# Optimization experiments

Measured on AMD Instinct MI355X. Metric: run time of the kernel, lower is better.

## Reference

```python
import jax, jax.numpy as jnp
import numpy as np

B = 262144   # batch
L = 50       # sequence feature length (hardcoded in source loop)
H = 1024     # fc_hidden_size
E = 256      # embedding_dim
DROP_P = 0.2


def setup_inputs() -> dict:
    key = jax.random.key(0)
    k1, k2, k3, k4 = jax.random.split(key, 4)
    seq = jax.random.normal(k1, (B, 1, L), dtype=jnp.float32)
    # emulate -1 padding after a random valid length so the early-break path is exercised
    lengths = jax.random.randint(k2, (B,), 10, L + 1)
    pad = jnp.arange(L)[None, None, :] >= lengths[:, None, None]
    seq = jnp.where(pad, jnp.float32(-1.0), seq)
    W1 = jax.random.normal(k3, (L, H), dtype=jnp.float32) * np.float32(1.0 / np.sqrt(L))
    b1 = jnp.zeros((H,), dtype=jnp.float32)
    W2 = jax.random.normal(k4, (H, E), dtype=jnp.float32) * np.float32(1.0 / np.sqrt(H))
    b2 = jnp.zeros((E,), dtype=jnp.float32)
    return {"seq": seq, "W1": W1, "b1": b1, "W2": W2, "b2": b2}


def reference(seq, W1, b1, W2, b2):
    x = seq[:, 0, :]                                   # [B, L]
    # first position equal to -1 per row (loop breaks there); L if none
    is_neg = x == jnp.float32(-1.0)
    first_neg = jnp.where(is_neg.any(axis=-1), jnp.argmax(is_neg, axis=-1), L)  # [B]
    valid = jnp.arange(L)[None, :] < first_neg[:, None]                          # [B, L]
    # per-element Bernoulli(0.2) dropout applied only before the break point
    drop = jax.random.uniform(jax.random.key(42), x.shape) < DROP_P
    x = jnp.where(drop & valid, jnp.float32(0.0), x)
    # Linear -> ReLU -> Linear, then squeeze(1) (already squeezed above)
    h = jax.nn.relu(x @ W1 + b1)                       # [B, H]
    return h @ W2 + b2                                 # [B, E]
```

## Files before the change

### kernel.cpp

```cpp
#include <hip/hip_runtime.h>


typedef __attribute__((ext_vector_type(8))) short short8;
typedef __attribute__((ext_vector_type(4))) float f32x4;

__device__ __forceinline__ unsigned short f2bf(float f) {
  unsigned u = __float_as_uint(f);
  u += 0x7fffu + ((u >> 16) & 1u);
  return (unsigned short)(u >> 16);
}

__device__ __forceinline__ unsigned rotl_(unsigned x, int d) {
  return (x << d) | (x >> (32 - d));
}

__device__ __forceinline__ bool drop_rand(unsigned j) {
  const unsigned k0 = 0u, k1 = 42u, k2 = 0x1BD11BDAu ^ 42u;
  unsigned v0 = 0u + k0;
  unsigned v1 = j + k1;
#define MIX(rot) { v0 += v1; v1 = rotl_(v1, rot); v1 ^= v0; }
  MIX(13) MIX(15) MIX(26) MIX(6)   v0 += k1; v1 += k2 + 1u;
  MIX(17) MIX(29) MIX(16) MIX(24)  v0 += k2; v1 += k0 + 2u;
  MIX(13) MIX(15) MIX(26) MIX(6)   v0 += k0; v1 += k1 + 3u;
  MIX(17) MIX(29) MIX(16) MIX(24)  v0 += k1; v1 += k2 + 4u;
  MIX(13) MIX(15) MIX(26) MIX(6)   v0 += k2; v1 += k0 + 5u;
#undef MIX
  unsigned bits = v0 ^ v1;
  float u = __uint_as_float((bits >> 9) | 0x3f800000u) - 1.0f;
  return u < 0.2f;
}

__global__ void pack_weights(const float* __restrict__ W1, const float* __restrict__ W2,
                             unsigned short* __restrict__ ws) {
  int t = blockIdx.x * 256 + threadIdx.x;
  if (t < 8192) {
    int nblk = t >> 7, kb = (t >> 6) & 1, lane = t & 63;
    int kbase = kb * 32 + ((lane >> 4) * 8);
    int col = nblk * 16 + (lane & 15);
    short8 vv;
#pragma unroll
    for (int j = 0; j < 8; ++j) {
      int k = kbase + j;
      vv[j] = (short)((k < 50) ? f2bf(W1[k * 1024 + col]) : (unsigned short)0);
    }
    *(short8*)&ws[t * 8] = vv;
  } else {
    int t2 = t - 8192;
    int c = t2 >> 11, kb = (t2 >> 10) & 1, nt = (t2 >> 6) & 15, lane = t2 & 63;
    int kbase = c * 64 + kb * 32 + ((lane >> 4) * 8);
    int e = nt * 16 + (lane & 15);
    short8 vv;
#pragma unroll
    for (int j = 0; j < 8; ++j) vv[j] = (short)f2bf(W2[(size_t)(kbase + j) * 256 + e]);
    *(short8*)&ws[65536 + t2 * 8] = vv;
  }
}

__global__ __launch_bounds__(512, 2) void mlp_fused(
    const float* __restrict__ seq, const float* __restrict__ b1,
    const float* __restrict__ b2, const unsigned short* __restrict__ ws,
    float* __restrict__ out) {
  __shared__ __align__(16) unsigned short lds_x[8192];
  __shared__ __align__(16) unsigned short lds_h[8192];
  __shared__ __align__(16) unsigned short lds_w2[16384];

  const int tid  = threadIdx.x;
  const int lane = tid & 63;
  const int wave = tid >> 6;
  const int quad = lane >> 4;
  const int l15  = lane & 15;
  const int m0   = blockIdx.x * 128;
  const unsigned short* pW1 = ws;
  const unsigned short* pW2 = ws + 65536;

  {
    int r = tid >> 2, q = tid & 3;
    int grow = m0 + r;
    const float* xrow = seq + (size_t)grow * 50;
    float xv[16];
    unsigned negm = 0;
#pragma unroll
    for (int i = 0; i < 16; ++i) {
      int l = q * 16 + i;
      float v = (l < 50) ? xrow[l] : 0.0f;
      xv[i] = v;
      if (v == -1.0f) negm |= (1u << i);
    }
    unsigned long long rm = ((unsigned long long)negm) << (q * 16);
    rm |= __shfl_xor(rm, 1);
    rm |= __shfl_xor(rm, 2);
    int fn = rm ? __builtin_ctzll(rm) : 64;
    unsigned jbase = (unsigned)grow * 50u;
#pragma unroll
    for (int g = 0; g < 2; ++g) {
      short8 vv;
#pragma unroll
      for (int i = 0; i < 8; ++i) {
        int l = q * 16 + g * 8 + i;
        float v = xv[g * 8 + i];
        if (l < fn && l < 50 && drop_rand(jbase + (unsigned)l)) v = 0.0f;
        vv[i] = (short)f2bf(v);
      }
      int kq = q * 2 + g;
      int idx = (((r >> 4) * 2 + (kq >> 2)) * 64 + (kq & 3) * 16 + (r & 15)) * 8;
      *(short8*)&lds_x[idx] = vv;
    }
  }

  f32x4 acc[4][4];
#pragma unroll
  for (int mi = 0; mi < 4; ++mi)
#pragma unroll
    for (int ni = 0; ni < 4; ++ni) acc[mi][ni] = f32x4{0.f, 0.f, 0.f, 0.f};

  const int w1m = wave >> 1, w1n = wave & 1;
  const int gm  = wave >> 2, gn  = wave & 3;

  for (int c = 0; c < 16; ++c) {
    short8 stg[4];
#pragma unroll
    for (int it = 0; it < 4; ++it)
      stg[it] = *(const short8*)&pW2[(size_t)c * 16384 + (size_t)(it * 512 + tid) * 8];

    __syncthreads();

    f32x4 hacc[2][2];
#pragma unroll
    for (int mi = 0; mi < 2; ++mi)
#pragma unroll
      for (int ni = 0; ni < 2; ++ni) hacc[mi][ni] = f32x4{0.f, 0.f, 0.f, 0.f};
#pragma unroll
    for (int kb = 0; kb < 2; ++kb) {
      short8 xa[2], wb[2];
#pragma unroll
      for (int mi = 0; mi < 2; ++mi)
        xa[mi] = *(const short8*)&lds_x[(size_t)(((w1m * 2 + mi) * 2 + kb) * 64 + lane) * 8];
#pragma unroll
      for (int ni = 0; ni < 2; ++ni)
        wb[ni] = *(const short8*)&pW1[(size_t)(((c * 4 + w1n * 2 + ni) * 2 + kb) * 64 + lane) * 8];
#pragma unroll
      for (int mi = 0; mi < 2; ++mi)
#pragma unroll
        for (int ni = 0; ni < 2; ++ni)
          hacc[mi][ni] = __builtin_amdgcn_mfma_f32_16x16x32_bf16(xa[mi], wb[ni], hacc[mi][ni], 0, 0, 0);
    }
#pragma unroll
    for (int ni = 0; ni < 2; ++ni) {
      int ntg = w1n * 2 + ni;
      int khl = ntg * 16 + l15;
      float b1v = b1[c * 64 + khl];
      int kb2 = ntg >> 1;
      int quad2 = ((ntg & 1) << 1) | (l15 >> 3);
      int jj = l15 & 7;
#pragma unroll
      for (int mi = 0; mi < 2; ++mi) {
        int mblk = w1m * 2 + mi;
#pragma unroll
        for (int r = 0; r < 4; ++r) {
          float v = fmaxf(hacc[mi][ni][r] + b1v, 0.0f);
          lds_h[(size_t)((mblk * 2 + kb2) * 64 + quad2 * 16 + quad * 4 + r) * 8 + jj] = f2bf(v);
        }
      }
    }
#pragma unroll
    for (int it = 0; it < 4; ++it)
      *(short8*)&lds_w2[(size_t)(it * 512 + tid) * 8] = stg[it];

    __syncthreads();

#pragma unroll
    for (int kb = 0; kb < 2; ++kb) {
      short8 ha[4], wb2[4];
#pragma unroll
      for (int mi = 0; mi < 4; ++mi)
        ha[mi] = *(const short8*)&lds_h[(size_t)(((gm * 4 + mi) * 2 + kb) * 64 + lane) * 8];
#pragma unroll
      for (int ni = 0; ni < 4; ++ni)
        wb2[ni] = *(const short8*)&lds_w2[(size_t)((kb * 16 + gn * 4 + ni) * 64 + lane) * 8];
#pragma unroll
      for (int mi = 0; mi < 4; ++mi)
#pragma unroll
        for (int ni = 0; ni < 4; ++ni)
          acc[mi][ni] = __builtin_amdgcn_mfma_f32_16x16x32_bf16(ha[mi], wb2[ni], acc[mi][ni], 0, 0, 0);
    }
  }

#pragma unroll
  for (int ni = 0; ni < 4; ++ni) {
    int e = (gn * 4 + ni) * 16 + l15;
    float b2v = b2[e];
#pragma unroll
    for (int mi = 0; mi < 4; ++mi) {
      int mrow = m0 + (gm * 4 + mi) * 16 + quad * 4;
#pragma unroll
      for (int r = 0; r < 4; ++r)
        out[(size_t)(mrow + r) * 256 + e] = acc[mi][ni][r] + b2v;
    }
  }
}

extern "C" void kernel_launch(void* const* d_in, const int* in_sizes, int n_in,
                              void* d_out, int out_size, void* d_ws, size_t ws_size,
                              hipStream_t stream) {
  const float* seq = (const float*)d_in[0];
  const float* W1  = (const float*)d_in[1];
  const float* b1  = (const float*)d_in[2];
  const float* W2  = (const float*)d_in[3];
  const float* b2  = (const float*)d_in[4];
  unsigned short* ws = (unsigned short*)d_ws;
  float* out = (float*)d_out;

  hipLaunchKernelGGL(pack_weights, dim3(160), dim3(256), 0, stream, W1, W2, ws);
  hipLaunchKernelGGL(mlp_fused, dim3(2048), dim3(512), 0, stream, seq, b1, b2, ws, out);
}
```

Baseline: 508.5 us.

## Keep X in registers, double-buffer H in LDS, read W2 directly from global

Each wave now keeps its own 16 input rows in registers and computes the full 64-wide hidden chunk as W1ᵀ·x, so the lds_x buffer goes away. The hidden tile is double-buffered in LDS, which cuts the per-chunk barriers from two to one. The W2 tile is no longer staged through LDS; each wave loads its W2 fragments straight from global memory and relies on L2/L1 hits. Less LDS lets the launch bounds target 4 blocks per CU, at the cost of more redundant global W2 traffic and possible register pressure from 16 accumulators.

```diff
diff --git a/kernel.cpp b/kernel.cpp
--- a/kernel.cpp
+++ b/kernel.cpp
@@ -56,145 +56,137 @@
   }
 }
 
-__global__ __launch_bounds__(512, 2) void mlp_fused(
+__global__ __launch_bounds__(512, 4) void mlp_fused(
     const float* __restrict__ seq, const float* __restrict__ b1,
     const float* __restrict__ b2, const unsigned short* __restrict__ ws,
     float* __restrict__ out) {
-  __shared__ __align__(16) unsigned short lds_x[8192];
-  __shared__ __align__(16) unsigned short lds_h[8192];
-  __shared__ __align__(16) unsigned short lds_w2[16384];
+  __shared__ __align__(16) unsigned short lds_h[2][8192];
 
   const int tid  = threadIdx.x;
   const int lane = tid & 63;
   const int wave = tid >> 6;
-  const int quad = lane >> 4;
+  const int q    = lane >> 4;
   const int l15  = lane & 15;
   const int m0   = blockIdx.x * 128;
   const unsigned short* pW1 = ws;
   const unsigned short* pW2 = ws + 65536;
 
+  short8 xb[2];
   {
-    int r = tid >> 2, q = tid & 3;
-    int grow = m0 + r;
-    const float* xrow = seq + (size_t)grow * 50;
-    float xv[16];
-    unsigned negm = 0;
-#pragma unroll
-    for (int i = 0; i < 16; ++i) {
-      int l = q * 16 + i;
-      float v = (l < 50) ? xrow[l] : 0.0f;
-      xv[i] = v;
-      if (v == -1.0f) negm |= (1u << i);
-    }
-    unsigned long long rm = ((unsigned long long)negm) << (q * 16);
-    rm |= __shfl_xor(rm, 1);
-    rm |= __shfl_xor(rm, 2);
-    int fn = rm ? __builtin_ctzll(rm) : 64;
-    unsigned jbase = (unsigned)grow * 50u;
-#pragma unroll
-    for (int g = 0; g < 2; ++g) {
+    const int row = m0 + wave * 16 + l15;
+    const float* xrow = seq + (size_t)row * 50;
+    float xv[2][8];
+    unsigned long long nm = 0ull;
+#pragma unroll
+    for (int kb = 0; kb < 2; ++kb) {
+#pragma unroll
+      for (int jp = 0; jp < 4; ++jp) {
+        const int k = kb * 32 + q * 8 + jp * 2;
+        float2 v;
+        if (k < 50) v = *(const float2*)&xrow[k];
+        else        v = make_float2(0.f, 0.f);
+        xv[kb][jp * 2]     = v.x;
+        xv[kb][jp * 2 + 1] = v.y;
+        if (v.x == -1.0f) nm |= 1ull << k;
+        if (v.y == -1.0f) nm |= 1ull << (k + 1);
+      }
+    }
+    nm |= __shfl_xor(nm, 16);
+    nm |= __shfl_xor(nm, 32);
+    const int fn   = nm ? __builtin_ctzll(nm) : 64;
+    const int kmax = fn < 50 ? fn : 50;
+    const unsigned jbase = (unsigned)row * 50u;
+#pragma unroll
+    for (int kb = 0; kb < 2; ++kb) {
       short8 vv;
 #pragma unroll
-      for (int i = 0; i < 8; ++i) {
-        int l = q * 16 + g * 8 + i;
-        float v = xv[g * 8 + i];
-        if (l < fn && l < 50 && drop_rand(jbase + (unsigned)l)) v = 0.0f;
-        vv[i] = (short)f2bf(v);
+      for (int j = 0; j < 8; ++j) {
+        const int k = kb * 32 + q * 8 + j;
+        float v = xv[kb][j];
+        if (k < kmax && drop_rand(jbase + (unsigned)k)) v = 0.0f;
+        vv[j] = (short)f2bf(v);
       }
-      int kq = q * 2 + g;
-      int idx = (((r >> 4) * 2 + (kq >> 2)) * 64 + (kq & 3) * 16 + (r & 15)) * 8;
-      *(short8*)&lds_x[idx] = vv;
-    }
-  }
-
-  f32x4 acc[4][4];
-#pragma unroll
-  for (int mi = 0; mi < 4; ++mi)
-#pragma unroll
-    for (int ni = 0; ni < 4; ++ni) acc[mi][ni] = f32x4{0.f, 0.f, 0.f, 0.f};
-
-  const int w1m = wave >> 1, w1n = wave & 1;
-  const int gm  = wave >> 2, gn  = wave & 3;
+      xb[kb] = vv;
+    }
+  }
+
+  f32x4 acc[2][8];
+#pragma unroll
+  for (int mt = 0; mt < 2; ++mt)
+#pragma unroll
+    for (int ni = 0; ni < 8; ++ni) acc[mt][ni] = f32x4{0.f, 0.f, 0.f, 0.f};
+
+  const int rg2 = wave >> 1;
+  const int cg  = wave & 1;
 
   for (int c = 0; c < 16; ++c) {
-    short8 stg[4];
-#pragma unroll
-    for (int it = 0; it < 4; ++it)
-      stg[it] = *(const short8*)&pW2[(size_t)c * 16384 + (size_t)(it * 512 + tid) * 8];
+    f32x4 hacc[4];
+#pragma unroll
+    for (int hi = 0; hi < 4; ++hi) hacc[hi] = f32x4{0.f, 0.f, 0.f, 0.f};
+#pragma unroll
+    for (int kb = 0; kb < 2; ++kb) {
+      short8 wa[4];
+#pragma unroll
+      for (int hi = 0; hi < 4; ++hi)
+        wa[hi] = *(const short8*)&pW1[(size_t)(((c * 4 + hi) * 2 + kb) * 64 + lane) * 8];
+#pragma unroll
+      for (int hi = 0; hi < 4; ++hi)
+        hacc[hi] = __builtin_amdgcn_mfma_f32_16x16x32_bf16(wa[hi], xb[kb], hacc[hi], 0, 0, 0);
+    }
+
+    unsigned short* hb = &lds_h[c & 1][0];
+#pragma unroll
+    for (int hi = 0; hi < 4; ++hi) {
+      const f32x4 bv = *(const f32x4*)&b1[c * 64 + hi * 16 + q * 4];
+      const float v0 = fmaxf(hacc[hi][0] + bv[0], 0.f);
+      const float v1 = fmaxf(hacc[hi][1] + bv[1], 0.f);
+      const float v2 = fmaxf(hacc[hi][2] + bv[2], 0.f);
+      const float v3 = fmaxf(hacc[hi][3] + bv[3], 0.f);
+      const unsigned w0 = (unsigned)f2bf(v0) | ((unsigned)f2bf(v1) << 16);
+      const unsigned w1 = (unsigned)f2bf(v2) | ((unsigned)f2bf(v3) << 16);
+      const int kb   = hi >> 1;
+      const int qp   = ((hi & 1) << 1) | (q >> 1);
+      const int elem = (wave * 2 + kb) * 64 + qp * 16 + l15;
+      uint2 val; val.x = w0; val.y = w1;
+      *(uint2*)&hb[elem * 8 + (q & 1) * 4] = val;
+    }
 
     __syncthreads();
 
-    f32x4 hacc[2][2];
-#pragma unroll
-    for (int mi = 0; mi < 2; ++mi)
-#pragma unroll
-      for (int ni = 0; ni < 2; ++ni) hacc[mi][ni] = f32x4{0.f, 0.f, 0.f, 0.f};
-#pragma unroll
-    for (int kb = 0; kb < 2; ++kb) {
-      short8 xa[2], wb[2];
-#pragma unroll
-      for (int mi = 0; mi < 2; ++mi)
-        xa[mi] = *(const short8*)&lds_x[(size_t)(((w1m * 2 + mi) * 2 + kb) * 64 + lane) * 8];
-#pragma unroll
-      for (int ni = 0; ni < 2; ++ni)
-        wb[ni] = *(const short8*)&pW1[(size_t)(((c * 4 + w1n * 2 + ni) * 2 + kb) * 64 + lane) * 8];
-#pragma unroll
-      for (int mi = 0; mi < 2; ++mi)
-#pragma unroll
-        for (int ni = 0; ni < 2; ++ni)
-          hacc[mi][ni] = __builtin_amdgcn_mfma_f32_16x16x32_bf16(xa[mi], wb[ni], hacc[mi][ni], 0, 0, 0);
-    }
-#pragma unroll
-    for (int ni = 0; ni < 2; ++ni) {
-      int ntg = w1n * 2 + ni;
-      int khl = ntg * 16 + l15;
-      float b1v = b1[c * 64 + khl];
-      int kb2 = ntg >> 1;
-      int quad2 = ((ntg & 1) << 1) | (l15 >> 3);
-      int jj = l15 & 7;
-#pragma unroll
-      for (int mi = 0; mi < 2; ++mi) {
-        int mblk = w1m * 2 + mi;
-#pragma unroll
-        for (int r = 0; r < 4; ++r) {
-          float v = fmaxf(hacc[mi][ni][r] + b1v, 0.0f);
-          lds_h[(size_t)((mblk * 2 + kb2) * 64 + quad2 * 16 + quad * 4 + r) * 8 + jj] = f2bf(v);
+#pragma unroll
+    for (int kb = 0; kb < 2; ++kb) {
+      short8 ha[2];
+#pragma unroll
+      for (int mt = 0; mt < 2; ++mt)
+        ha[mt] = *(const short8*)&lds_h[c & 1][(size_t)(((rg2 * 2 + mt) * 2 + kb) * 64 + lane) * 8];
+#pragma unroll
+      for (int ng = 0; ng < 2; ++ng) {
+        short8 wb[4];
+#pragma unroll
+        for (int ni = 0; ni < 4; ++ni) {
+          const int nt = cg * 8 + ng * 4 + ni;
+          wb[ni] = *(const short8*)&pW2[(size_t)(((c * 2 + kb) * 16 + nt) * 64 + lane) * 8];
         }
+#pragma unroll
+        for (int mt = 0; mt < 2; ++mt)
+#pragma unroll
+          for (int ni = 0; ni < 4; ++ni)
+            acc[mt][ng * 4 + ni] =
+                __builtin_amdgcn_mfma_f32_16x16x32_bf16(ha[mt], wb[ni], acc[mt][ng * 4 + ni], 0, 0, 0);
       }
     }
-#pragma unroll
-    for (int it = 0; it < 4; ++it)
-      *(short8*)&lds_w2[(size_t)(it * 512 + tid) * 8] = stg[it];
-
-    __syncthreads();
-
-#pragma unroll
-    for (int kb = 0; kb < 2; ++kb) {
-      short8 ha[4], wb2[4];
-#pragma unroll
-      for (int mi = 0; mi < 4; ++mi)
-        ha[mi] = *(const short8*)&lds_h[(size_t)(((gm * 4 + mi) * 2 + kb) * 64 + lane) * 8];
-#pragma unroll
-      for (int ni = 0; ni < 4; ++ni)
-        wb2[ni] = *(const short8*)&lds_w2[(size_t)((kb * 16 + gn * 4 + ni) * 64 + lane) * 8];
-#pragma unroll
-      for (int mi = 0; mi < 4; ++mi)
-#pragma unroll
-        for (int ni = 0; ni < 4; ++ni)
-          acc[mi][ni] = __builtin_amdgcn_mfma_f32_16x16x32_bf16(ha[mi], wb2[ni], acc[mi][ni], 0, 0, 0);
-    }
-  }
-
-#pragma unroll
-  for (int ni = 0; ni < 4; ++ni) {
-    int e = (gn * 4 + ni) * 16 + l15;
-    float b2v = b2[e];
-#pragma unroll
-    for (int mi = 0; mi < 4; ++mi) {
-      int mrow = m0 + (gm * 4 + mi) * 16 + quad * 4;
+  }
+
+#pragma unroll
+  for (int ng = 0; ng < 8; ++ng) {
+    const int e = cg * 128 + ng * 16 + l15;
+    const float b2v = b2[e];
+#pragma unroll
+    for (int mt = 0; mt < 2; ++mt) {
+      const int rbase = m0 + rg2 * 32 + mt * 16 + q * 4;
 #pragma unroll
       for (int r = 0; r < 4; ++r)
-        out[(size_t)(mrow + r) * 256 + e] = acc[mi][ni][r] + b2v;
+        out[(size_t)(rbase + r) * 256 + e] = acc[mt][ng][r] + b2v;
     }
   }
 }
```

Result: slower. 792.8 us (+55.9%).
